# Performance work log

Measured on AMD Instinct MI355X. Metric: run time of the kernel, lower is better.

The kernel has to match this reference:

```python
import jax, jax.numpy as jnp
import numpy as np

K, B, T, D = 4, 4096, 32, 128


def setup_inputs() -> dict:
    key = jax.random.key(0)
    k1, k2, k3 = jax.random.split(key, 3)
    semb = jax.random.normal(k1, (K, B, D), dtype=jnp.float32)
    slabels = jax.random.randint(k2, (K, B), 0, 2, dtype=jnp.int32)
    topk_ngh = jax.random.randint(k3, (K, B, T), 0, B, dtype=jnp.int32)
    return {"semb": semb, "slabels": slabels, "topk_ngh": topk_ngh}


def reference(semb, slabels, topk_ngh):
    """Dense, masked reformulation of DistanceLayer.forward (hardest=False).

    Original emits, per domain k and anchor i, one triplet for every pair
    (sn, dn) where sn/dn are topk neighbors of i with same/different binary
    label, carrying sim[i,sn] (pos_dist), sim[i,dn] (neg_dist) and the anchor/
    pos/neg embeddings. Here we return the same quantities densified over the
    fixed [K,B,T,T] pair grid with a validity mask (jit-compatible shapes).
    Anchor embeddings are semb itself; pos/neg embeddings are rows of
    nbr_embed selected by the same/diff sides of pair_mask.
    """
    gather = jax.vmap(lambda tbl, idx: tbl[idx])  # per-domain row gather
    nbr_embed = gather(semb, topk_ngh)            # [K,B,T,D]
    nbr_label = gather(slabels, topk_ngh)         # [K,B,T]
    # sim[i, ngh[i,t]] without materializing the full [B,B] sim matrix
    nsim = jnp.einsum('kbd,kbtd->kbt', semb, nbr_embed)  # [K,B,T]
    same = nbr_label == slabels[:, :, None]       # neighbor shares anchor label
    pair_mask = same[:, :, :, None] & (~same)[:, :, None, :]  # [K,B,T,T]
    pos_dist = jnp.where(pair_mask, nsim[:, :, :, None], 0.0)  # sim(i, sn)
    neg_dist = jnp.where(pair_mask, nsim[:, :, None, :], 0.0)  # sim(i, dn)
    return pos_dist, neg_dist, pair_mask, nbr_embed
```

## Files before the change

### kernel.cpp

```cpp
#include <hip/hip_runtime.h>
#include <hip/hip_bf16.h>

constexpr int K = 4;
constexpr int B = 4096;
constexpr int T = 32;
constexpr int D = 128;
constexpr int TT = T * T;
constexpr int TD = T * D;

typedef float f4 __attribute__((ext_vector_type(4)));

__device__ __forceinline__ float dot4(f4 a, f4 b) {
    return a.x * b.x + a.y * b.y + a.z * b.z + a.w * b.w;
}

__device__ __forceinline__ float hreduce32(float p) {
    #pragma unroll
    for (int m = 16; m >= 1; m >>= 1) p += __shfl_xor(p, m, 64);
    return p;
}

__global__ __launch_bounds__(256) void distance_layer_kernel(
    const float* __restrict__ semb,
    const int*   __restrict__ slabels,
    const int*   __restrict__ topk,
    float* __restrict__ pos,
    float* __restrict__ neg,
    float* __restrict__ maskf,
    float* __restrict__ nbr)
{
    const int kb  = blockIdx.x;
    const int k   = kb >> 12;
    const int tid = threadIdx.x;

    __shared__ f4    anchor4[T];
    __shared__ int   idx_s[T];
    __shared__ float nsim_s[T];
    __shared__ int   same_s[T];

    const int my_label = slabels[kb];
    if (tid < T) {
        const int idx = topk[kb * T + tid];
        idx_s[tid]  = idx;
        same_s[tid] = (slabels[(k << 12) + idx] == my_label) ? 1 : 0;
        anchor4[tid] =
            reinterpret_cast<const f4*>(semb + (size_t)kb * D)[tid];
    }
    __syncthreads();

    const f4* semb4 = reinterpret_cast<const f4*>(semb + (size_t)k * B * D);
    f4*       nbr4  = reinterpret_cast<f4*>(nbr + (size_t)kb * TD);

    const int w  = tid >> 5;
    const int d4 = tid & 31;
    const f4  a  = anchor4[d4];
    const int i0 = idx_s[w], i1 = idx_s[8 + w], i2 = idx_s[16 + w], i3 = idx_s[24 + w];

    const f4 s0 = semb4[(size_t)i0 * (D / 4) + d4];
    const f4 s1 = semb4[(size_t)i1 * (D / 4) + d4];
    const f4 s2 = semb4[(size_t)i2 * (D / 4) + d4];
    const f4 s3 = semb4[(size_t)i3 * (D / 4) + d4];
    nbr4[(0  + w) * (D / 4) + d4] = s0;
    nbr4[(8  + w) * (D / 4) + d4] = s1;
    nbr4[(16 + w) * (D / 4) + d4] = s2;
    nbr4[(24 + w) * (D / 4) + d4] = s3;

    const float p0 = hreduce32(dot4(a, s0));
    const float p1 = hreduce32(dot4(a, s1));
    const float p2 = hreduce32(dot4(a, s2));
    const float p3 = hreduce32(dot4(a, s3));
    if (d4 == 0) {
        nsim_s[0  + w] = p0;
        nsim_s[8  + w] = p1;
        nsim_s[16 + w] = p2;
        nsim_s[24 + w] = p3;
    }
    __syncthreads();

    f4* pos4  = reinterpret_cast<f4*>(pos   + (size_t)kb * TT);
    f4* neg4  = reinterpret_cast<f4*>(neg   + (size_t)kb * TT);
    f4* mask4 = reinterpret_cast<f4*>(maskf + (size_t)kb * TT);

    const int s_row = tid >> 3;
    const int d0    = (tid & 7) * 4;
    const int   ss = same_s[s_row];
    const float ps = nsim_s[s_row];

    f4 pv, nv, mv;
    {
        const int m0 = ss & (same_s[d0 + 0] ^ 1);
        const int m1 = ss & (same_s[d0 + 1] ^ 1);
        const int m2 = ss & (same_s[d0 + 2] ^ 1);
        const int m3 = ss & (same_s[d0 + 3] ^ 1);
        pv.x = m0 ? ps : 0.0f;  nv.x = m0 ? nsim_s[d0 + 0] : 0.0f;  mv.x = (float)m0;
        pv.y = m1 ? ps : 0.0f;  nv.y = m1 ? nsim_s[d0 + 1] : 0.0f;  mv.y = (float)m1;
        pv.z = m2 ? ps : 0.0f;  nv.z = m2 ? nsim_s[d0 + 2] : 0.0f;  mv.z = (float)m2;
        pv.w = m3 ? ps : 0.0f;  nv.w = m3 ? nsim_s[d0 + 3] : 0.0f;  mv.w = (float)m3;
    }
    pos4[tid]  = pv;
    neg4[tid]  = nv;
    mask4[tid] = mv;
}

extern "C" void kernel_launch(void* const* d_in, const int* in_sizes, int n_in,
                              void* d_out, int out_size, void* d_ws, size_t ws_size,
                              hipStream_t stream) {
    const float* semb    = (const float*)d_in[0];
    const int*   slabels = (const int*)d_in[1];
    const int*   topk    = (const int*)d_in[2];

    float* out = (float*)d_out;
    const size_t KBTT = (size_t)K * B * T * T;
    float* pos   = out;
    float* neg   = out + KBTT;
    float* maskf = out + 2 * KBTT;
    float* nbr   = out + 3 * KBTT;

    distance_layer_kernel<<<dim3(K * B), dim3(256), 0, stream>>>(
        semb, slabels, topk, pos, neg, maskf, nbr);
}
```

Measured before the change: 459.3 us.

## Assign one anchor per wavefront and drop block-level barriers

Each 64-lane wavefront now handles one (domain, anchor) pair, so a 256-thread block processes four anchors. The kernel drops both __syncthreads. Neighbor indices are spread across lanes with shuffles, the same-label flags are packed into a ballot bitmask, and each lane issues 8 gathered row loads per group instead of 4. This aims to remove barrier stalls and raise memory-level parallelism on a kernel bound by output writes. The trade-off is a quarter as many blocks, more registers per thread, and reliance on ordering within a wavefront for the LDS nsim exchange.

```diff
diff --git a/kernel.cpp b/kernel.cpp
--- a/kernel.cpp
+++ b/kernel.cpp
@@ -1,5 +1,4 @@
 #include <hip/hip_runtime.h>
-#include <hip/hip_bf16.h>
 
 constexpr int K = 4;
 constexpr int B = 4096;
@@ -20,6 +19,8 @@
     return p;
 }
 
+struct __align__(16) WaveSh { float nsim[T]; };
+
 __global__ __launch_bounds__(256) void distance_layer_kernel(
     const float* __restrict__ semb,
     const int*   __restrict__ slabels,
@@ -29,77 +30,81 @@
     float* __restrict__ maskf,
     float* __restrict__ nbr)
 {
-    const int kb  = blockIdx.x;
-    const int k   = kb >> 12;
-    const int tid = threadIdx.x;
+    const int tid  = threadIdx.x;
+    const int wid  = tid >> 6;
+    const int l    = tid & 63;
+    const int half = l >> 5;
+    const int d4   = l & 31;
 
-    __shared__ f4    anchor4[T];
-    __shared__ int   idx_s[T];
-    __shared__ float nsim_s[T];
-    __shared__ int   same_s[T];
+    const int kb = blockIdx.x * 4 + wid;
+    const int k  = kb >> 12;
+
+    __shared__ WaveSh sh[4];
+    WaveSh& w = sh[wid];
 
     const int my_label = slabels[kb];
-    if (tid < T) {
-        const int idx = topk[kb * T + tid];
-        idx_s[tid]  = idx;
-        same_s[tid] = (slabels[(k << 12) + idx] == my_label) ? 1 : 0;
-        anchor4[tid] =
-            reinterpret_cast<const f4*>(semb + (size_t)kb * D)[tid];
-    }
-    __syncthreads();
+    const int idx_l    = topk[kb * T + d4];
+    const int same_l   = (slabels[(k << 12) + idx_l] == my_label) ? 1 : 0;
+    const unsigned mask = (unsigned)__ballot(same_l);
 
     const f4* semb4 = reinterpret_cast<const f4*>(semb + (size_t)k * B * D);
     f4*       nbr4  = reinterpret_cast<f4*>(nbr + (size_t)kb * TD);
+    const f4  a     = reinterpret_cast<const f4*>(semb + (size_t)kb * D)[d4];
 
-    const int w  = tid >> 5;
-    const int d4 = tid & 31;
-    const f4  a  = anchor4[d4];
-    const int i0 = idx_s[w], i1 = idx_s[8 + w], i2 = idx_s[16 + w], i3 = idx_s[24 + w];
+    #pragma unroll
+    for (int g = 0; g < 2; ++g) {
+        int ridx[8];
+        #pragma unroll
+        for (int j = 0; j < 8; ++j)
+            ridx[j] = __shfl(idx_l, 16 * g + 2 * j + half, 64);
 
-    const f4 s0 = semb4[(size_t)i0 * (D / 4) + d4];
-    const f4 s1 = semb4[(size_t)i1 * (D / 4) + d4];
-    const f4 s2 = semb4[(size_t)i2 * (D / 4) + d4];
-    const f4 s3 = semb4[(size_t)i3 * (D / 4) + d4];
-    nbr4[(0  + w) * (D / 4) + d4] = s0;
-    nbr4[(8  + w) * (D / 4) + d4] = s1;
-    nbr4[(16 + w) * (D / 4) + d4] = s2;
-    nbr4[(24 + w) * (D / 4) + d4] = s3;
+        f4 sv[8];
+        #pragma unroll
+        for (int j = 0; j < 8; ++j)
+            sv[j] = semb4[(size_t)ridx[j] * (D / 4) + d4];
 
-    const float p0 = hreduce32(dot4(a, s0));
-    const float p1 = hreduce32(dot4(a, s1));
-    const float p2 = hreduce32(dot4(a, s2));
-    const float p3 = hreduce32(dot4(a, s3));
-    if (d4 == 0) {
-        nsim_s[0  + w] = p0;
-        nsim_s[8  + w] = p1;
-        nsim_s[16 + w] = p2;
-        nsim_s[24 + w] = p3;
+        #pragma unroll
+        for (int j = 0; j < 8; ++j) {
+            const int row = 16 * g + 2 * j + half;
+            nbr4[row * (D / 4) + d4] = sv[j];
+            const float p = hreduce32(dot4(a, sv[j]));
+            if (d4 == 0) w.nsim[row] = p;
+        }
     }
-    __syncthreads();
+
+    const int d0 = (l & 7) * 4;
+    const f4 ndv = *reinterpret_cast<const f4*>(&w.nsim[d0]);
+    const unsigned md = (mask >> d0) & 0xFu;
+    const int b0 =  md       & 1;
+    const int b1 = (md >> 1) & 1;
+    const int b2 = (md >> 2) & 1;
+    const int b3 = (md >> 3) & 1;
 
     f4* pos4  = reinterpret_cast<f4*>(pos   + (size_t)kb * TT);
     f4* neg4  = reinterpret_cast<f4*>(neg   + (size_t)kb * TT);
     f4* mask4 = reinterpret_cast<f4*>(maskf + (size_t)kb * TT);
 
-    const int s_row = tid >> 3;
-    const int d0    = (tid & 7) * 4;
-    const int   ss = same_s[s_row];
-    const float ps = nsim_s[s_row];
+    #pragma unroll
+    for (int i = 0; i < 4; ++i) {
+        const int   s  = 8 * i + (l >> 3);
+        const int   ss = (mask >> s) & 1;
+        const float ps = w.nsim[s];
 
-    f4 pv, nv, mv;
-    {
-        const int m0 = ss & (same_s[d0 + 0] ^ 1);
-        const int m1 = ss & (same_s[d0 + 1] ^ 1);
-        const int m2 = ss & (same_s[d0 + 2] ^ 1);
-        const int m3 = ss & (same_s[d0 + 3] ^ 1);
-        pv.x = m0 ? ps : 0.0f;  nv.x = m0 ? nsim_s[d0 + 0] : 0.0f;  mv.x = (float)m0;
-        pv.y = m1 ? ps : 0.0f;  nv.y = m1 ? nsim_s[d0 + 1] : 0.0f;  mv.y = (float)m1;
-        pv.z = m2 ? ps : 0.0f;  nv.z = m2 ? nsim_s[d0 + 2] : 0.0f;  mv.z = (float)m2;
-        pv.w = m3 ? ps : 0.0f;  nv.w = m3 ? nsim_s[d0 + 3] : 0.0f;  mv.w = (float)m3;
+        const int m0 = ss & (b0 ^ 1);
+        const int m1 = ss & (b1 ^ 1);
+        const int m2 = ss & (b2 ^ 1);
+        const int m3 = ss & (b3 ^ 1);
+
+        f4 pv, nv, mv;
+        pv.x = m0 ? ps : 0.0f;  nv.x = m0 ? ndv.x : 0.0f;  mv.x = (float)m0;
+        pv.y = m1 ? ps : 0.0f;  nv.y = m1 ? ndv.y : 0.0f;  mv.y = (float)m1;
+        pv.z = m2 ? ps : 0.0f;  nv.z = m2 ? ndv.z : 0.0f;  mv.z = (float)m2;
+        pv.w = m3 ? ps : 0.0f;  nv.w = m3 ? ndv.w : 0.0f;  mv.w = (float)m3;
+
+        pos4 [64 * i + l] = pv;
+        neg4 [64 * i + l] = nv;
+        mask4[64 * i + l] = mv;
     }
-    pos4[tid]  = pv;
-    neg4[tid]  = nv;
-    mask4[tid] = mv;
 }
 
 extern "C" void kernel_launch(void* const* d_in, const int* in_sizes, int n_in,
@@ -116,6 +121,6 @@
     float* maskf = out + 2 * KBTT;
     float* nbr   = out + 3 * KBTT;
 
-    distance_layer_kernel<<<dim3(K * B), dim3(256), 0, stream>>>(
+    distance_layer_kernel<<<dim3(K * B / 4), dim3(256), 0, stream>>>(
         semb, slabels, topk, pos, neg, maskf, nbr);
 }
```

New measurement: 463.6 us (median of 2 runs). About the same (+0.9%).
